# Optimization experiments

Hardware: AMD Instinct MI355X
Metric: run time of the kernel (lower is better)

Reference implementation:

```python
import jax, jax.numpy as jnp
import numpy as np


def setup_inputs() -> dict:
    key = jax.random.key(0)
    k1, k2, k3, k4 = jax.random.split(key, 4)
    B, c_in, N, L = 32, 64, 512, 64
    K, c_out = 3, 64
    x = jax.random.normal(k1, (B, c_in, N, L), dtype=jnp.float32)
    adj = jax.random.uniform(k2, (N, N), dtype=jnp.float32)
    ds = jax.random.uniform(k3, (B, N, N), dtype=jnp.float32)
    W = jax.random.normal(k4, (c_out, K * c_in), dtype=jnp.float32) * 0.02
    b = jnp.zeros((c_out,), dtype=jnp.float32)
    return {"x": x, "adj": adj, "ds": ds, "W": W, "b": b}


def reference(x, adj, ds, W, b):
    B, c_in, N, L = x.shape
    K = W.shape[1] // c_in
    I = jnp.eye(N, dtype=x.dtype)
    # Chebyshev polynomial recurrence T_k(adj), each scaled per-sample by ds
    Ls = [ds * I, ds * adj]          # each [B, N, N]
    L0, L1 = I, adj
    for _ in range(2, K):
        L2 = 2.0 * (adj @ L1) - L0
        L0, L1 = L1, L2
        Ls.append(ds * L2)
    Lap = jnp.stack(Ls, axis=1)      # [B, K, N, N]
    Lap = jnp.swapaxes(Lap, -1, -2)  # transpose(-1, -2)
    # bcnl, bknq -> bckql : contract over node axis n
    xk = jnp.einsum('bcnl,bknq->bckql', x, Lap)
    xk = xk.reshape(B, c_in * K, N, L)
    # 1x1 Conv2d == channel-mixing matmul
    out = jnp.einsum('bfnl,of->bonl', xk, W) + b[None, :, None, None]
    return out
```

## Files before the change

kernel.cpp:

```cpp
#include <hip/hip_runtime.h>
#include <stdint.h>

typedef __bf16 bf16x8 __attribute__((ext_vector_type(8)));
typedef float  f32x4  __attribute__((ext_vector_type(4)));

#define AS1 __attribute__((address_space(1)))
#define AS3 __attribute__((address_space(3)))

__device__ __forceinline__ void gload_lds16(const void* g, void* l) {
    __builtin_amdgcn_global_load_lds((const AS1 uint32_t*)g, (AS3 uint32_t*)l, 16, 0, 0);
}

__device__ __forceinline__ float bf2f(unsigned short u) {
    union { unsigned int i; float f; } v; v.i = ((unsigned int)u) << 16; return v.f;
}


__global__ __launch_bounds__(256) void k_t2(const float* __restrict__ adj,
                                            float* __restrict__ T2f) {
    const int q = blockIdx.x, tx = threadIdx.x;
    float a0 = 0.f, a1 = 0.f;
    for (int m = 0; m < 512; ++m) {
        const float av = adj[q*512 + m];
        a0 += av * adj[m*512 + tx];
        a1 += av * adj[m*512 + tx + 256];
    }
    T2f[q*512 + tx      ] = 2.f*a0 - ((q == tx      ) ? 1.f : 0.f);
    T2f[q*512 + tx + 256] = 2.f*a1 - ((q == tx + 256) ? 1.f : 0.f);
}

__global__ __launch_bounds__(256) void k_w2(const float* __restrict__ W,
                                            __bf16* __restrict__ W2bf) {
    const int t = blockIdx.x*256 + threadIdx.x;
    const int f = t >> 6, c = t & 63;
    const int k = f >> 6, o = f & 63;
    W2bf[t] = (__bf16)W[o*192 + c*3 + k];
}

__global__ __launch_bounds__(256) void k_abuild(const float* __restrict__ ds,
                                                const float* __restrict__ adj,
                                                const float* __restrict__ T2f,
                                                __bf16* __restrict__ Abf,
                                                float* __restrict__ dsd, int b0) {
    const int bx = blockIdx.x;
    const int bb = bx >> 9, q = bx & 511;
    const int b  = b0 + bb;
    const float* dsr  = ds  + ((size_t)b*512 + q)*512;
    __bf16*      arow = Abf + ((size_t)bb*512 + q)*1024;
    if (threadIdx.x == 0) dsd[bb*512 + q] = dsr[q];
    for (int j = threadIdx.x; j < 1024; j += 256) {
        const int n = j & 511;
        const float tv = (j < 512) ? adj[q*512 + n] : T2f[q*512 + n];
        arow[j] = (__bf16)(dsr[n] * tv);
    }
}

__global__ __launch_bounds__(256) void k_zprep(const float* __restrict__ x,
                                               const __bf16* __restrict__ W2bf,
                                               __bf16* __restrict__ zT, int b0) {
    __shared__ __align__(16) char lds_raw[52224];
    __bf16* W2s = (__bf16*)lds_raw;
    __bf16* Xs  = (__bf16*)(lds_raw + 27648);
    __bf16* Dsh = (__bf16*)lds_raw;

    const int t = threadIdx.x, lane = t & 63, w = t >> 6;
    const int nb = gridDim.x;
    int bx = blockIdx.x;
    bx = (bx & 7) * (nb >> 3) + (bx >> 3);
    const int bb = bx >> 8;  const int r = bx & 255;
    const int ng = r >> 4, lg = r & 15;
    const int l0 = lg*4, n0 = ng*32;
    const int b  = b0 + bb;

    #pragma unroll
    for (int i = 0; i < 6; ++i) {
        const int u = t + 256*i, f = u >> 3, seg = u & 7;
        *(bf16x8*)(W2s + f*72 + seg*8) = *(const bf16x8*)(W2bf + f*64 + seg*8);
    }
    #pragma unroll
    for (int p = 0; p < 8; ++p) {
        const int u = t + 256*p, c = u >> 5, nn = u & 31;
        const float4 v = *(const float4*)(x + (((size_t)b*64 + c)*512 + (n0 + nn))*64 + l0);
        Xs[(nn     )*72 + c] = (__bf16)v.x;
        Xs[(nn + 32)*72 + c] = (__bf16)v.y;
        Xs[(nn + 64)*72 + c] = (__bf16)v.z;
        Xs[(nn + 96)*72 + c] = (__bf16)v.w;
    }
    __syncthreads();

    f32x4 acc[3][8] = {};
    const int fw = w*48, m15 = lane & 15, quad = lane >> 4;
    #pragma unroll
    for (int ks = 0; ks < 2; ++ks) {
        const int c0 = ks*32 + quad*8;
        bf16x8 a[3], bv[8];
        #pragma unroll
        for (int i = 0; i < 3; ++i)
            a[i] = *(const bf16x8*)(W2s + (fw + i*16 + m15)*72 + c0);
        #pragma unroll
        for (int j = 0; j < 8; ++j)
            bv[j] = *(const bf16x8*)(Xs + (j*16 + m15)*72 + c0);
        #pragma unroll
        for (int i = 0; i < 3; ++i)
            #pragma unroll
            for (int j = 0; j < 8; ++j)
                acc[i][j] = __builtin_amdgcn_mfma_f32_16x16x32_bf16(a[i], bv[j], acc[i][j], 0, 0, 0);
    }
    __syncthreads();

    #pragma unroll
    for (int i = 0; i < 3; ++i)
        #pragma unroll
        for (int j = 0; j < 8; ++j) {
            const int f = fw + i*16 + quad*4, m = j*16 + m15;
            #pragma unroll
            for (int rr = 0; rr < 4; ++rr)
                Dsh[(f + rr)*136 + m] = (__bf16)acc[i][j][rr];
        }
    __syncthreads();

    #pragma unroll
    for (int i = 0; i < 3; ++i) {
        const int u = t + 256*i, f = u >> 2, lp = u & 3;
        const int k = f >> 6, o = f & 63;
        __bf16* dst = zT + ((size_t)bb*4096 + o*64 + (l0 + lp))*1536 + k*512 + n0;
        const __bf16* srcp = Dsh + f*136 + lp*32;
        *(bf16x8*)(dst +  0) = *(const bf16x8*)(srcp +  0);
        *(bf16x8*)(dst +  8) = *(const bf16x8*)(srcp +  8);
        *(bf16x8*)(dst + 16) = *(const bf16x8*)(srcp + 16);
        *(bf16x8*)(dst + 24) = *(const bf16x8*)(srcp + 24);
    }
}

__global__ __launch_bounds__(256) void k_gemm(const __bf16* __restrict__ Abf,
                                              const __bf16* __restrict__ zT,
                                              const float* __restrict__ dsd,
                                              const float* __restrict__ bias,
                                              float* __restrict__ out, int b0) {
    __shared__ __align__(16) __bf16 As[2][128*32];
    __shared__ __align__(16) __bf16 Bs[2][128*32];
    const int t = threadIdx.x, lane = t & 63, w = t >> 6;
    const int nb = gridDim.x;
    int bx = blockIdx.x;
    bx = (bx & 7) * (nb >> 3) + (bx >> 3);
    const int bb = bx >> 7;  const int r = bx & 127;
    const int qt = r & 3, ft = r >> 2;
    const int q0 = qt*128, f20 = ft*128;
    const __bf16* Ab = Abf + (size_t)bb*512 *1024;
    const __bf16* Bb = zT  + (size_t)bb*4096*1536;
    const int lrow = lane >> 2, lseg = lane & 3;
    const int m15 = lane & 15, quad = lane >> 4;
    const int wq = (w >> 1)*64, wf = (w & 1)*64;
    const int rb0 = w*32;

    f32x4 acc[4][4] = {};

    auto stage = [&](int buf, int it) {
        const int j0 = it * 32;
        #pragma unroll
        for (int i = 0; i < 2; ++i) {
            const int rb = rb0 + i*16;
            gload_lds16(Ab + (size_t)(q0  + rb + lrow)*1024 + j0       + lseg*8, &As[buf][rb*32]);
            gload_lds16(Bb + (size_t)(f20 + rb + lrow)*1536 + 512 + j0 + lseg*8, &Bs[buf][rb*32]);
        }
    };
    auto compute = [&](int buf) {
        bf16x8 av[4], bv[4];
        const int co = quad*8;
        #pragma unroll
        for (int i = 0; i < 4; ++i) av[i] = *(const bf16x8*)(&As[buf][(wq + i*16 + m15)*32 + co]);
        #pragma unroll
        for (int j = 0; j < 4; ++j) bv[j] = *(const bf16x8*)(&Bs[buf][(wf + j*16 + m15)*32 + co]);
        #pragma unroll
        for (int i = 0; i < 4; ++i)
            #pragma unroll
            for (int j = 0; j < 4; ++j)
                acc[i][j] = __builtin_amdgcn_mfma_f32_16x16x32_bf16(av[i], bv[j], acc[i][j], 0, 0, 0);
    };

    stage(0, 0);
    __syncthreads();
    int cur = 0;
    for (int it = 0; it < 31; ++it) {
        stage(cur ^ 1, it + 1);
        compute(cur);
        __syncthreads();
        cur ^= 1;
    }
    compute(cur);

    const float* dsdb = dsd + bb*512;
    #pragma unroll
    for (int i = 0; i < 4; ++i) {
        const int qb = q0 + wq + i*16 + quad*4;
        const float4 dv = *(const float4*)(dsdb + qb);
        #pragma unroll
        for (int j = 0; j < 4; ++j) {
            const int f2 = f20 + wf + j*16 + m15;
            const ushort4 zv = *(const ushort4*)((const unsigned short*)Bb + (size_t)f2*1536 + qb);
            acc[i][j][0] += dv.x * bf2f(zv.x);
            acc[i][j][1] += dv.y * bf2f(zv.y);
            acc[i][j][2] += dv.z * bf2f(zv.z);
            acc[i][j][3] += dv.w * bf2f(zv.w);
        }
    }

    const int b = b0 + bb;
    #pragma unroll
    for (int j = 0; j < 4; ++j) {
        const int f2 = f20 + wf + j*16 + m15;
        const int o = f2 >> 6, l = f2 & 63;
        const float bi = bias[o];
        #pragma unroll
        for (int i = 0; i < 4; ++i) {
            const int qb = q0 + wq + i*16 + quad*4;
            float* dst = out + (((size_t)b*64 + o)*512 + qb)*64 + l;
            dst[  0] = acc[i][j][0] + bi;
            dst[ 64] = acc[i][j][1] + bi;
            dst[128] = acc[i][j][2] + bi;
            dst[192] = acc[i][j][3] + bi;
        }
    }
}

extern "C" void kernel_launch(void* const* d_in, const int* in_sizes, int n_in,
                              void* d_out, int out_size, void* d_ws, size_t ws_size,
                              hipStream_t stream) {
    (void)in_sizes; (void)n_in; (void)out_size;
    const float* x    = (const float*)d_in[0];
    const float* adj  = (const float*)d_in[1];
    const float* ds   = (const float*)d_in[2];
    const float* W    = (const float*)d_in[3];
    const float* bias = (const float*)d_in[4];
    float* out = (float*)d_out;
    char*  ws  = (char*)d_ws;

    float*  T2f  = (float*)ws;
    __bf16* W2bf = (__bf16*)(ws + (1u << 20));
    float*  dsd  = (float*)(ws + (1u << 20) + 32768);
    char*   chunk0 = ws + (1u << 20) + 32768 + 65536;

    const size_t abytes = (size_t)512 *1024*2;
    const size_t zbytes = (size_t)4096*1536*2;
    const size_t perb   = abytes + zbytes;
    const size_t head   = (1u << 20) + 32768 + 65536;

    int bpc = 1;
    if (ws_size > head) {
        size_t a = (ws_size - head) / perb;
        bpc = (a < 1) ? 1 : (a > 32 ? 32 : (int)a);
    }

    k_t2<<<dim3(512), dim3(256), 0, stream>>>(adj, T2f);
    k_w2<<<dim3(48),  dim3(256), 0, stream>>>(W, W2bf);

    __bf16* Abf = (__bf16*)chunk0;
    __bf16* zTp = (__bf16*)(chunk0 + (size_t)bpc*abytes);
    for (int b0 = 0; b0 < 32; b0 += bpc) {
        const int bc = (32 - b0 < bpc) ? (32 - b0) : bpc;
        k_abuild<<<dim3(bc*512), dim3(256), 0, stream>>>(ds, adj, T2f, Abf, dsd, b0);
        k_zprep <<<dim3(bc*256), dim3(256), 0, stream>>>(x, W2bf, zTp, b0);
        k_gemm  <<<dim3(bc*128), dim3(256), 0, stream>>>(Abf, zTp, dsd, bias, out, b0);
    }
}
```

Measured before the change: 944.7 us.

## Load GEMM operands directly from global into registers, dropping LDS staging

The GEMM kernel no longer double-buffers A and B tiles in shared memory through global_load_lds. Each wave now reads its MFMA fragments straight from global memory and unrolls the loop four times. This removes LDS traffic and the per-iteration barriers, at the cost of losing reuse across waves: each A and B fragment is loaded by two waves, which doubles global/L2 traffic. Latency hiding now depends on the compiler's unrolled prefetching rather than an explicit pipeline.

```diff
diff --git a/kernel.cpp b/kernel.cpp
--- a/kernel.cpp
+++ b/kernel.cpp
@@ -6,10 +6,6 @@
 
 #define AS1 __attribute__((address_space(1)))
 #define AS3 __attribute__((address_space(3)))
-
-__device__ __forceinline__ void gload_lds16(const void* g, void* l) {
-    __builtin_amdgcn_global_load_lds((const AS1 uint32_t*)g, (AS3 uint32_t*)l, 16, 0, 0);
-}
 
 __device__ __forceinline__ float bf2f(unsigned short u) {
     union { unsigned int i; float f; } v; v.i = ((unsigned int)u) << 16; return v.f;
@@ -137,8 +133,6 @@
                                               const float* __restrict__ dsd,
                                               const float* __restrict__ bias,
                                               float* __restrict__ out, int b0) {
-    __shared__ __align__(16) __bf16 As[2][128*32];
-    __shared__ __align__(16) __bf16 Bs[2][128*32];
     const int t = threadIdx.x, lane = t & 63, w = t >> 6;
     const int nb = gridDim.x;
     int bx = blockIdx.x;
@@ -148,46 +142,27 @@
     const int q0 = qt*128, f20 = ft*128;
     const __bf16* Ab = Abf + (size_t)bb*512 *1024;
     const __bf16* Bb = zT  + (size_t)bb*4096*1536;
-    const int lrow = lane >> 2, lseg = lane & 3;
     const int m15 = lane & 15, quad = lane >> 4;
     const int wq = (w >> 1)*64, wf = (w & 1)*64;
-    const int rb0 = w*32;
+
+    const __bf16* pa = Ab + (size_t)(q0 + wq + m15)*1024 + quad*8;
+    const __bf16* pb = Bb + (size_t)(f20 + wf + m15)*1536 + 512 + quad*8;
 
     f32x4 acc[4][4] = {};
-
-    auto stage = [&](int buf, int it) {
-        const int j0 = it * 32;
-        #pragma unroll
-        for (int i = 0; i < 2; ++i) {
-            const int rb = rb0 + i*16;
-            gload_lds16(Ab + (size_t)(q0  + rb + lrow)*1024 + j0       + lseg*8, &As[buf][rb*32]);
-            gload_lds16(Bb + (size_t)(f20 + rb + lrow)*1536 + 512 + j0 + lseg*8, &Bs[buf][rb*32]);
-        }
-    };
-    auto compute = [&](int buf) {
+    #pragma unroll 4
+    for (int it = 0; it < 32; ++it) {
         bf16x8 av[4], bv[4];
-        const int co = quad*8;
-        #pragma unroll
-        for (int i = 0; i < 4; ++i) av[i] = *(const bf16x8*)(&As[buf][(wq + i*16 + m15)*32 + co]);
-        #pragma unroll
-        for (int j = 0; j < 4; ++j) bv[j] = *(const bf16x8*)(&Bs[buf][(wf + j*16 + m15)*32 + co]);
+        #pragma unroll
+        for (int i = 0; i < 4; ++i) av[i] = *(const bf16x8*)(pa + i*16*1024);
+        #pragma unroll
+        for (int j = 0; j < 4; ++j) bv[j] = *(const bf16x8*)(pb + j*16*1536);
         #pragma unroll
         for (int i = 0; i < 4; ++i)
             #pragma unroll
             for (int j = 0; j < 4; ++j)
                 acc[i][j] = __builtin_amdgcn_mfma_f32_16x16x32_bf16(av[i], bv[j], acc[i][j], 0, 0, 0);
-    };
-
-    stage(0, 0);
-    __syncthreads();
-    int cur = 0;
-    for (int it = 0; it < 31; ++it) {
-        stage(cur ^ 1, it + 1);
-        compute(cur);
-        __syncthreads();
-        cur ^= 1;
-    }
-    compute(cur);
+        pa += 32; pb += 32;
+    }
 
     const float* dsdb = dsd + bb*512;
     #pragma unroll
```

Measured after the change: 1.190 ms. 1.26x slower.
